# Kernel tuning notes

Hardware: AMD Instinct MI355X
Metric: run time of the kernel (lower is better)

The kernel has to match this reference:

```python
import jax, jax.numpy as jnp
import numpy as np

C = 64
K = 3          # kernel_size
EK = 5         # encoder_kernel
PAD = (K - 1) // 2


def _conv(x, w, pad):
    return jax.lax.conv_general_dilated(
        x, w, window_strides=(1, 1), padding=[(pad, pad), (pad, pad)],
        dimension_numbers=('NCHW', 'OIHW', 'NCHW'))


def setup_inputs() -> dict:
    key = jax.random.key(0)
    ks = jax.random.split(key, 6)
    b, h, w = 8, 128, 128
    x = jax.random.normal(ks[0], (b, C, h, w), dtype=jnp.float32)
    # gen_kernel: 1x1 conv (C->C, with bias) then EKxEK conv (C->K*K, no bias)
    w1 = jax.random.normal(ks[1], (C, C, 1, 1), dtype=jnp.float32) * (1.0 / np.sqrt(C))
    b1 = jax.random.normal(ks[2], (C,), dtype=jnp.float32) * 0.01
    w2 = jax.random.normal(ks[3], (K * K, C, EK, EK), dtype=jnp.float32) * (1.0 / np.sqrt(C * EK * EK))
    # consensus t_c: 1x1 conv C->C//4, relu, 1x1 conv C//4->C, relu (no bias)
    tc1 = jax.random.normal(ks[4], (C // 4, C, 1, 1), dtype=jnp.float32) * (1.0 / np.sqrt(C))
    tc2 = jax.random.normal(ks[5], (C, C // 4, 1, 1), dtype=jnp.float32) * (1.0 / np.sqrt(C // 4))
    return {"x": x, "w1": w1, "b1": b1, "w2": w2, "tc1": tc1, "tc2": tc2}


def reference(x, w1, b1, w2, tc1, tc2):
    b, c, h, w = x.shape
    oh, ow = h, w  # stride == 1
    # dynamic kernel logits: (b, K*K, oh, ow)
    y = _conv(x, w1, 0) + b1[None, :, None, None]
    wt = _conv(y, w2, (EK - 1) // 2)
    # consensus scale: adaptive avg pool to 1x1 then mean over batch -> (c,)
    x_con = jnp.mean(x, axis=(0, 2, 3))                      # (c,)
    h1 = jax.nn.relu(jnp.einsum('oc,c->o', tc1[:, :, 0, 0], x_con))
    tmp = jax.nn.relu(jnp.einsum('oc,c->o', tc2[:, :, 0, 0], h1))  # (c,)
    # broadcast logits to (b, c, K*K, oh, ow) and softmax over K*K
    logits = wt[:, None, :, :, :] * tmp[None, :, None, None, None]
    attn = jax.nn.softmax(logits, axis=2)                    # (b,c,9,oh,ow)
    # unfold patches: reflect-pad then 9 shifted views, order kh*K+kw (row-major)
    px = jnp.pad(x, ((0, 0), (0, 0), (PAD, PAD), (PAD, PAD)), mode='reflect')
    pats = jnp.stack([px[:, :, i:i + oh, j:j + ow]
                      for i in range(K) for j in range(K)], axis=2)  # (b,c,9,oh,ow)
    out = jnp.sum(attn * pats, axis=2)                       # (b,c,oh,ow)
    return out
```

## Files before the change

### kernel.cpp

```cpp
#include <hip/hip_runtime.h>
#include <hip/hip_bf16.h>
#include <cstddef>


#define B 8
#define C 64
#define HW 128
#define NK 9
#define NT 25
#define LOG2E 1.4426950408889634f
#define PSTR 72

typedef __attribute__((ext_vector_type(8))) short short8;
typedef __attribute__((ext_vector_type(4))) float float4v;
typedef __attribute__((ext_vector_type(4))) unsigned int uint4v;

__device__ __forceinline__ unsigned short f2bf(float f) {
    unsigned int u = __float_as_uint(f);
    unsigned int r = u + 0x7FFF + ((u >> 16) & 1);
    return (unsigned short)(r >> 16);
}
__device__ __forceinline__ float fast_exp2(float x) {
    float r;
    asm("v_exp_f32 %0, %1" : "=v"(r) : "v"(x));
    return r;
}
__device__ __forceinline__ float fast_rcp(float x) {
    float r;
    asm("v_rcp_f32 %0, %1" : "=v"(r) : "v"(x));
    return r;
}

__global__ __launch_bounds__(256) void transpose_kernel(const float* __restrict__ x,
                                                        unsigned short* __restrict__ xT,
                                                        float* __restrict__ part) {
    __shared__ float tile[64 * 129];
    const int gi = blockIdx.x, b = blockIdx.y;
    const int tid = threadIdx.x;
    for (int it = 0; it < 8; ++it) {
        const int idx = it * 256 + tid;
        const int cidx = idx >> 5, f4 = idx & 31;
        float4 v = *(const float4*)(x + (((size_t)(b * C + cidx)) * HW + gi) * HW + f4 * 4);
        tile[cidx * 129 + f4 * 4 + 0] = v.x;
        tile[cidx * 129 + f4 * 4 + 1] = v.y;
        tile[cidx * 129 + f4 * 4 + 2] = v.z;
        tile[cidx * 129 + f4 * 4 + 3] = v.w;
    }
    __syncthreads();
    for (int it = 0; it < 4; ++it) {
        const int idx = it * 256 + tid;
        const int gj = idx >> 3, c8 = idx & 7;
        unsigned int p[4];
#pragma unroll
        for (int s = 0; s < 4; ++s) {
            unsigned int lo = f2bf(tile[(c8 * 8 + 2 * s) * 129 + gj]);
            unsigned int hi = f2bf(tile[(c8 * 8 + 2 * s + 1) * 129 + gj]);
            p[s] = lo | (hi << 16);
        }
        uint4v outv = {p[0], p[1], p[2], p[3]};
        *(uint4v*)(xT + (((size_t)b * (HW * HW) + gi * HW + gj) * C + c8 * 8)) = outv;
    }
    if (tid < 64) {
        float s = 0.f;
        for (int g = 0; g < 128; ++g) s += tile[tid * 129 + g];
        atomicAdd(part + tid, s);
    }
}

__global__ __launch_bounds__(256) void prep_kernel(const float* __restrict__ w1,
                                                   const float* __restrict__ b1,
                                                   const float* __restrict__ w2,
                                                   unsigned short* __restrict__ Abuf,
                                                   float* __restrict__ betaG) {
    if (blockIdx.x < 50) {
        __shared__ float sw2[NK * 64];
        __shared__ float sw1[64 * 32];
        const int chunk = blockIdx.x;
        const int t = chunk >> 1, ch = chunk & 1;
        for (int idx = threadIdx.x; idx < NK * 64; idx += 256) {
            const int m = idx >> 6, cc = idx & 63;
            sw2[idx] = w2[(m * 64 + cc) * NT + t];
        }
        for (int idx = threadIdx.x; idx < 2048; idx += 256) {
            const int cc = idx >> 5, j = idx & 31;
            sw1[idx] = w1[cc * 64 + ch * 32 + j];
        }
        __syncthreads();
        for (int sidx = 0; sidx < 2; ++sidx) {
            const int slot = sidx * 256 + threadIdx.x;
            const int quad = slot >> 7, m = (slot >> 3) & 15, jj = slot & 7;
            unsigned short hi = 0, lo = 0;
            if (m < NK) {
                float s = 0.f;
                for (int cc = 0; cc < 64; ++cc)
                    s += sw2[m * 64 + cc] * sw1[cc * 32 + quad * 8 + jj];
                hi = f2bf(s);
                lo = f2bf(s - __uint_as_float(((unsigned int)hi) << 16));
            }
            Abuf[chunk * 1024 + slot] = hi;
            Abuf[chunk * 1024 + 512 + slot] = lo;
        }
    } else {
        __shared__ float beta_s[NT * NK];
        const int t0 = threadIdx.x;
        if (t0 < NT * NK) {
            const int t = t0 / NK, k = t0 - t * NK;
            float s = 0.f;
            for (int cc = 0; cc < 64; ++cc)
                s += w2[(k * 64 + cc) * NT + t] * b1[cc];
            beta_s[t0] = s;
        }
        __syncthreads();
        if (t0 < 225) {
            const int ic = t0 / 45, jc = (t0 / 9) % 5, k = t0 % 9;
            float s = 0.f;
            for (int eh = 0; eh < 5; ++eh) {
                bool rok = (ic == 0) ? (eh >= 2) : (ic == 1) ? (eh >= 1)
                          : (ic == 3) ? (eh <= 3) : (ic == 4) ? (eh <= 2) : true;
                if (!rok) continue;
                for (int ew = 0; ew < 5; ++ew) {
                    bool cok = (jc == 0) ? (ew >= 2) : (jc == 1) ? (ew >= 1)
                              : (jc == 3) ? (ew <= 3) : (jc == 4) ? (ew <= 2) : true;
                    if (cok) s += beta_s[(eh * 5 + ew) * NK + k];
                }
            }
            betaG[t0] = s;
        }
    }
}

__global__ __launch_bounds__(512, 4) void fused_kernel(const unsigned short* __restrict__ xT,
                                                       const unsigned short* __restrict__ Abuf,
                                                       const float* __restrict__ betaG,
                                                       const float* __restrict__ part,
                                                       const float* __restrict__ tc1,
                                                       const float* __restrict__ tc2,
                                                       float* __restrict__ out) {
    __shared__ unsigned short stag[400 * PSTR];
    __shared__ float wpart[128 * 10];
    __shared__ float lt[C];
    const int b = blockIdx.y;
    const int i0 = (blockIdx.x >> 3) * 16, j0 = (blockIdx.x & 7) * 16;
    const int tid = threadIdx.x, lane = tid & 63, wid = tid >> 6;
    const int n = lane & 15, q = lane >> 4;
    const int rowg = wid >> 1, h = wid & 1;

    for (int idx = tid; idx < 3200; idx += 512) {
        const int pix = idx >> 3, g8 = idx & 7;
        const int li = pix / 20, lj = pix - li * 20;
        const int gi = i0 + li - 2, gj = j0 + lj - 2;
        uint4v v = {0u, 0u, 0u, 0u};
        if (gi >= 0 && gi < HW && gj >= 0 && gj < HW)
            v = *(const uint4v*)(xT + (((size_t)b * (HW * HW) + gi * HW + gj) * C + g8 * 8));
        *(uint4v*)(stag + pix * PSTR + g8 * 8) = v;
    }

    if (wid == 0) {
        float xcv = part[lane] * (1.f / (B * HW * HW));
        float hh = 0.f;
        for (int c = 0; c < C; ++c) {
            float xcc = __shfl(xcv, c);
            if (lane < 16) hh += tc1[lane * C + c] * xcc;
        }
        hh = fmaxf(hh, 0.f);
        float ltv = 0.f;
#pragma unroll
        for (int o = 0; o < 16; ++o) {
            float ho = __shfl(hh, o);
            ltv += tc2[lane * 16 + o] * ho;
        }
        lt[lane] = fmaxf(ltv, 0.f) * LOG2E;
    }

    const int prow = rowg * 4 + q, pcol = n;
    const int pgi = i0 + prow, pgj = j0 + pcol;
    float bgv[NK];
    if (h == 0) {
        const int ic = pgi < 2 ? pgi : (pgi > 125 ? pgi - 123 : 2);
        const int jc = pgj < 2 ? pgj : (pgj > 125 ? pgj - 123 : 2);
        const float* bp = betaG + (ic * 5 + jc) * NK;
#pragma unroll
        for (int k = 0; k < NK; ++k) bgv[k] = bp[k];
    }

    __syncthreads();

    float4v acc[4];
    const float4v zero4 = {0.f, 0.f, 0.f, 0.f};
#pragma unroll
    for (int g = 0; g < 4; ++g) acc[g] = zero4;

    const unsigned short* Ab = Abuf + h * 1024 + lane * 8;
    const unsigned short* sb = stag + h * 32 + q * 8;
#pragma unroll
    for (int eh = 0; eh < 5; ++eh) {
#pragma unroll
        for (int ew = 0; ew < 5; ++ew) {
            const int t = eh * 5 + ew;
            const short8 ahi = *(const short8*)(Ab + t * 2048);
            const short8 alo = *(const short8*)(Ab + t * 2048 + 512);
#pragma unroll
            for (int g = 0; g < 4; ++g) {
                const int r = rowg * 4 + g;
                const short8 bf = *(const short8*)(sb + ((r + eh) * 20 + ew + n) * PSTR);
                acc[g] = __builtin_amdgcn_mfma_f32_16x16x32_bf16(ahi, bf, acc[g], 0, 0, 0);
                acc[g] = __builtin_amdgcn_mfma_f32_16x16x32_bf16(alo, bf, acc[g], 0, 0, 0);
            }
        }
    }

    float wv[NK];
#pragma unroll
    for (int k = 0; k < NK; ++k) {
        const int src = (k >> 2) * 16 + n;
        const int rr = k & 3;
        float v0 = __shfl(acc[0][rr], src);
        float v1 = __shfl(acc[1][rr], src);
        float v2 = __shfl(acc[2][rr], src);
        float v3 = __shfl(acc[3][rr], src);
        wv[k] = (q == 0) ? v0 : (q == 1) ? v1 : (q == 2) ? v2 : v3;
    }

    const int lp = ((rowg & 1) << 6) + lane;
    for (int pg = 0; pg < 2; ++pg) {
        const bool inpass = (rowg >> 1) == pg;
        if (pg) __syncthreads();
        if (inpass && h == 1) {
#pragma unroll
            for (int k = 0; k < NK; ++k) wpart[lp * 10 + k] = wv[k];
        }
        __syncthreads();
        if (inpass && h == 0) {
            float w9[NK];
            float wmax = -1e30f;
#pragma unroll
            for (int k = 0; k < NK; ++k) {
                w9[k] = wv[k] + wpart[lp * 10 + k] + bgv[k];
                wmax = fmaxf(wmax, w9[k]);
            }
#pragma unroll
            for (int k = 0; k < NK; ++k) wpart[lp * 10 + k] = w9[k] - wmax;
        }
        __syncthreads();
#pragma unroll
        for (int s = 0; s < 2; ++s) {
            const int task = tid * 2 + s;
            const int lpx = task >> 3, oct = task & 7;
            const int l6 = lpx & 63;
            const int brow = (2 * pg + (lpx >> 6)) * 4 + (l6 >> 4);
            const int bcol = l6 & 15;
            const int bgi = i0 + brow, bgj = j0 + bcol;
            float dv[NK];
#pragma unroll
            for (int k = 0; k < NK; ++k) dv[k] = wpart[lpx * 10 + k];
            int r0 = bgi - 1; r0 = r0 < 0 ? 1 : r0;
            int r2 = bgi + 1; r2 = r2 > 127 ? 126 : r2;
            int c0 = bgj - 1; c0 = c0 < 0 ? 1 : c0;
            int c2 = bgj + 1; c2 = c2 > 127 ? 126 : c2;
            const int R[3] = {r0 - i0 + 2, bgi - i0 + 2, r2 - i0 + 2};
            const int Cc[3] = {c0 - j0 + 2, bgj - j0 + 2, c2 - j0 + 2};
            const unsigned short* sb2 = stag + oct * 8;
            uint4v xs[NK];
#pragma unroll
            for (int kh = 0; kh < 3; ++kh)
#pragma unroll
                for (int kw = 0; kw < 3; ++kw)
                    xs[kh * 3 + kw] = *(const uint4v*)(sb2 + (R[kh] * 20 + Cc[kw]) * PSTR);
            float* outp = out + (((size_t)b * C + oct * 8) * HW + bgi) * HW + bgj;
#pragma unroll
            for (int jj = 0; jj < 4; ++jj) {
                const float t0 = lt[oct * 8 + jj * 2];
                const float t1 = lt[oct * 8 + jj * 2 + 1];
                float s0 = 0.f, o0 = 0.f, s1 = 0.f, o1 = 0.f;
#pragma unroll
                for (int k = 0; k < NK; ++k) {
                    const unsigned int u = xs[k][jj];
                    const float e0 = fast_exp2(dv[k] * t0);
                    const float e1 = fast_exp2(dv[k] * t1);
                    s0 += e0; o0 = fmaf(e0, __uint_as_float(u << 16), o0);
                    s1 += e1; o1 = fmaf(e1, __uint_as_float(u & 0xffff0000u), o1);
                }
                outp[(size_t)(jj * 2) * (HW * HW)] = o0 * fast_rcp(s0);
                outp[(size_t)(jj * 2 + 1) * (HW * HW)] = o1 * fast_rcp(s1);
            }
        }
    }
}

extern "C" void kernel_launch(void* const* d_in, const int* in_sizes, int n_in,
                              void* d_out, int out_size, void* d_ws, size_t ws_size,
                              hipStream_t stream) {
    const float* x   = (const float*)d_in[0];
    const float* w1  = (const float*)d_in[1];
    const float* b1  = (const float*)d_in[2];
    const float* w2  = (const float*)d_in[3];
    const float* tc1 = (const float*)d_in[4];
    const float* tc2 = (const float*)d_in[5];
    float* out = (float*)d_out;

    char* ws = (char*)d_ws;
    float* part  = (float*)(ws + 0);
    unsigned short* Abuf = (unsigned short*)(ws + 1024);
    float* betaG = (float*)(ws + 103424);
    unsigned short* xT = (unsigned short*)(ws + 104448);

    hipMemsetAsync(part, 0, 64 * sizeof(float), stream);
    prep_kernel<<<51, 256, 0, stream>>>(w1, b1, w2, Abuf, betaG);
    transpose_kernel<<<dim3(HW, B), 256, 0, stream>>>(x, xT, part);
    fused_kernel<<<dim3(64, B), 512, 0, stream>>>(xT, Abuf, betaG, part, tc1, tc2, out);
}
```

Baseline: 156.0 us.

## Drop bf16 transpose pass; stage NCHW x directly into LDS inside fused kernel

Removes the separate transpose kernel that wrote a channel-last bf16 copy of x. The fused kernel now reads fp32 NCHW x directly, converts it to bf16 and scatters it into the LDS staging tile. The channel mean moves to a dedicated reduction kernel that writes per-quarter partial sums, which also removes the memset and atomics. The MFMA loop is reordered so each ew column loads its 8 B-fragments into registers once and reuses them across eh, cutting LDS reads at the cost of more registers and 2-byte scattered LDS stores.

```diff
diff --git a/kernel.cpp b/kernel.cpp
--- a/kernel.cpp
+++ b/kernel.cpp
@@ -31,40 +31,26 @@
     return r;
 }
 
-__global__ __launch_bounds__(256) void transpose_kernel(const float* __restrict__ x,
-                                                        unsigned short* __restrict__ xT,
-                                                        float* __restrict__ part) {
-    __shared__ float tile[64 * 129];
-    const int gi = blockIdx.x, b = blockIdx.y;
-    const int tid = threadIdx.x;
-    for (int it = 0; it < 8; ++it) {
-        const int idx = it * 256 + tid;
-        const int cidx = idx >> 5, f4 = idx & 31;
-        float4 v = *(const float4*)(x + (((size_t)(b * C + cidx)) * HW + gi) * HW + f4 * 4);
-        tile[cidx * 129 + f4 * 4 + 0] = v.x;
-        tile[cidx * 129 + f4 * 4 + 1] = v.y;
-        tile[cidx * 129 + f4 * 4 + 2] = v.z;
-        tile[cidx * 129 + f4 * 4 + 3] = v.w;
-    }
+__global__ __launch_bounds__(256) void xcon_kernel(const float* __restrict__ x,
+                                                   float* __restrict__ part) {
+    const int c = blockIdx.x >> 2, qb = blockIdx.x & 3;
+    float s = 0.f;
+    for (int bb = 0; bb < 2; ++bb) {
+        const int b = qb * 2 + bb;
+        const float4* p = (const float4*)(x + ((size_t)(b * C + c)) * (HW * HW));
+        for (int idx = threadIdx.x; idx < (HW * HW) / 4; idx += 256) {
+            float4 v = p[idx];
+            s += (v.x + v.y) + (v.z + v.w);
+        }
+    }
+    __shared__ float red[256];
+    red[threadIdx.x] = s;
     __syncthreads();
-    for (int it = 0; it < 4; ++it) {
-        const int idx = it * 256 + tid;
-        const int gj = idx >> 3, c8 = idx & 7;
-        unsigned int p[4];
-#pragma unroll
-        for (int s = 0; s < 4; ++s) {
-            unsigned int lo = f2bf(tile[(c8 * 8 + 2 * s) * 129 + gj]);
-            unsigned int hi = f2bf(tile[(c8 * 8 + 2 * s + 1) * 129 + gj]);
-            p[s] = lo | (hi << 16);
-        }
-        uint4v outv = {p[0], p[1], p[2], p[3]};
-        *(uint4v*)(xT + (((size_t)b * (HW * HW) + gi * HW + gj) * C + c8 * 8)) = outv;
-    }
-    if (tid < 64) {
-        float s = 0.f;
-        for (int g = 0; g < 128; ++g) s += tile[tid * 129 + g];
-        atomicAdd(part + tid, s);
-    }
+    for (int off = 128; off > 0; off >>= 1) {
+        if (threadIdx.x < off) red[threadIdx.x] += red[threadIdx.x + off];
+        __syncthreads();
+    }
+    if (threadIdx.x == 0) part[c * 4 + qb] = red[0];
 }
 
 __global__ __launch_bounds__(256) void prep_kernel(const float* __restrict__ w1,
@@ -129,7 +115,7 @@
     }
 }
 
-__global__ __launch_bounds__(512, 4) void fused_kernel(const unsigned short* __restrict__ xT,
+__global__ __launch_bounds__(512, 4) void fused_kernel(const float* __restrict__ x,
                                                        const unsigned short* __restrict__ Abuf,
                                                        const float* __restrict__ betaG,
                                                        const float* __restrict__ part,
@@ -145,18 +131,25 @@
     const int n = lane & 15, q = lane >> 4;
     const int rowg = wid >> 1, h = wid & 1;
 
-    for (int idx = tid; idx < 3200; idx += 512) {
-        const int pix = idx >> 3, g8 = idx & 7;
-        const int li = pix / 20, lj = pix - li * 20;
-        const int gi = i0 + li - 2, gj = j0 + lj - 2;
-        uint4v v = {0u, 0u, 0u, 0u};
-        if (gi >= 0 && gi < HW && gj >= 0 && gj < HW)
-            v = *(const uint4v*)(xT + (((size_t)b * (HW * HW) + gi * HW + gj) * C + g8 * 8));
-        *(uint4v*)(stag + pix * PSTR + g8 * 8) = v;
+    for (int idx = tid; idx < 12800; idx += 512) {
+        const int ch = idx / 200;
+        const int rem = idx - ch * 200;
+        const int li = rem / 10, cp = rem - li * 10;
+        const int gi = i0 + li - 2;
+        const int gj = j0 + cp * 2 - 2;
+        unsigned int pack = 0u;
+        if (gi >= 0 && gi < HW && gj >= 0 && gj <= HW - 2) {
+            const float2 v = *(const float2*)(x + (((size_t)(b * C + ch)) * HW + gi) * HW + gj);
+            pack = (unsigned int)f2bf(v.x) | ((unsigned int)f2bf(v.y) << 16);
+        }
+        const int p0 = (li * 20 + cp * 2) * PSTR + ch;
+        stag[p0] = (unsigned short)(pack & 0xffffu);
+        stag[p0 + PSTR] = (unsigned short)(pack >> 16);
     }
 
     if (wid == 0) {
-        float xcv = part[lane] * (1.f / (B * HW * HW));
+        float xcv = (part[lane * 4 + 0] + part[lane * 4 + 1]
+                   + part[lane * 4 + 2] + part[lane * 4 + 3]) * (1.f / (B * HW * HW));
         float hh = 0.f;
         for (int c = 0; c < C; ++c) {
             float xcc = __shfl(xcv, c);
@@ -172,8 +165,8 @@
         lt[lane] = fmaxf(ltv, 0.f) * LOG2E;
     }
 
-    const int prow = rowg * 4 + q, pcol = n;
-    const int pgi = i0 + prow, pgj = j0 + pcol;
+    const int prow = rowg * 4 + q;
+    const int pgi = i0 + prow, pgj = j0 + n;
     float bgv[NK];
     if (h == 0) {
         const int ic = pgi < 2 ? pgi : (pgi > 125 ? pgi - 123 : 2);
@@ -193,18 +186,20 @@
     const unsigned short* Ab = Abuf + h * 1024 + lane * 8;
     const unsigned short* sb = stag + h * 32 + q * 8;
 #pragma unroll
-    for (int eh = 0; eh < 5; ++eh) {
-#pragma unroll
-        for (int ew = 0; ew < 5; ++ew) {
+    for (int ew = 0; ew < 5; ++ew) {
+        short8 w8[8];
+#pragma unroll
+        for (int rr = 0; rr < 8; ++rr)
+            w8[rr] = *(const short8*)(sb + ((rowg * 4 + rr) * 20 + ew + n) * PSTR);
+#pragma unroll
+        for (int eh = 0; eh < 5; ++eh) {
             const int t = eh * 5 + ew;
             const short8 ahi = *(const short8*)(Ab + t * 2048);
             const short8 alo = *(const short8*)(Ab + t * 2048 + 512);
 #pragma unroll
             for (int g = 0; g < 4; ++g) {
-                const int r = rowg * 4 + g;
-                const short8 bf = *(const short8*)(sb + ((r + eh) * 20 + ew + n) * PSTR);
-                acc[g] = __builtin_amdgcn_mfma_f32_16x16x32_bf16(ahi, bf, acc[g], 0, 0, 0);
-                acc[g] = __builtin_amdgcn_mfma_f32_16x16x32_bf16(alo, bf, acc[g], 0, 0, 0);
+                acc[g] = __builtin_amdgcn_mfma_f32_16x16x32_bf16(ahi, w8[g + eh], acc[g], 0, 0, 0);
+                acc[g] = __builtin_amdgcn_mfma_f32_16x16x32_bf16(alo, w8[g + eh], acc[g], 0, 0, 0);
             }
         }
     }
@@ -302,10 +297,8 @@
     float* part  = (float*)(ws + 0);
     unsigned short* Abuf = (unsigned short*)(ws + 1024);
     float* betaG = (float*)(ws + 103424);
-    unsigned short* xT = (unsigned short*)(ws + 104448);
-
-    hipMemsetAsync(part, 0, 64 * sizeof(float), stream);
+
+    xcon_kernel<<<256, 256, 0, stream>>>(x, part);
     prep_kernel<<<51, 256, 0, stream>>>(w1, b1, w2, Abuf, betaG);
-    transpose_kernel<<<dim3(HW, B), 256, 0, stream>>>(x, xT, part);
-    fused_kernel<<<dim3(64, B), 512, 0, stream>>>(xT, Abuf, betaG, part, tc1, tc2, out);
-}
+    fused_kernel<<<dim3(64, B), 512, 0, stream>>>(x, Abuf, betaG, part, tc1, tc2, out);
+}
```

Result: faster. 149.0 us (-4.5%).
